# Kernel optimization log

Hardware: AMD Instinct MI355X
Metric: run time of the kernel (lower is better)

Reference implementation:

```python
import jax, jax.numpy as jnp
import numpy as np
import math

N, E, H, A = 50000, 800000, 128, 8
D = H // A


def setup_inputs() -> dict:
    key = jax.random.key(0)
    ks = jax.random.split(key, 12)
    q = jax.random.normal(ks[0], (N, H), dtype=jnp.float32)
    k = jax.random.normal(ks[1], (N, H), dtype=jnp.float32)
    v = jax.random.normal(ks[2], (N, H), dtype=jnp.float32)
    Wq = jax.random.normal(ks[3], (H, H), dtype=jnp.float32) * 0.05
    bq = jax.random.normal(ks[4], (H,), dtype=jnp.float32) * 0.05
    Wk = jax.random.normal(ks[5], (H, H), dtype=jnp.float32) * 0.05
    bk = jax.random.normal(ks[6], (H,), dtype=jnp.float32) * 0.05
    Wv = jax.random.normal(ks[7], (H, H), dtype=jnp.float32) * 0.05
    bv = jax.random.normal(ks[8], (H,), dtype=jnp.float32) * 0.05
    # Ensure every node id appears at least once in q_indices so that
    # q_indices.unique() == arange(N) and the output shape is static [N, H].
    tail = jax.random.randint(ks[9], (E - N,), 0, N)
    q_indices = jnp.concatenate([jnp.arange(N), tail]).astype(jnp.int32)
    k_indices = jax.random.randint(ks[10], (E,), 0, N).astype(jnp.int32)
    return {"q": q, "k": k, "v": v, "Wq": Wq, "bq": bq, "Wk": Wk, "bk": bk,
            "Wv": Wv, "bv": bv, "q_indices": q_indices, "k_indices": k_indices}


def reference(q, k, v, Wq, bq, Wk, bk, Wv, bv, q_indices, k_indices):
    n = q.shape[0]
    # Gather node features per edge (irregular access).
    qe = q[q_indices]            # [E, H]
    ke = k[k_indices]            # [E, H]
    ve = v[k_indices]            # [E, H]
    # Linear projections (torch Linear: x @ W.T + b), split heads -> [E, A, D].
    Q = (qe @ Wq.T + bq).reshape(-1, A, D)
    K = (ke @ Wk.T + bk).reshape(-1, A, D)
    V = (ve @ Wv.T + bv).reshape(-1, A, D)
    # Per-edge scaled dot-product scores: [E, A].
    scores = jnp.einsum('ead,ead->ea', Q, K) / math.sqrt(D)
    # Segment softmax over edges sharing the same destination node
    # (faithful to the original: plain exp, no max subtraction).
    ex = jnp.exp(scores)                                        # [E, A]
    denom = jax.ops.segment_sum(ex, q_indices, num_segments=n)  # [N, A]
    probs = ex / denom[q_indices]                               # [E, A]
    # Scatter-aggregate weighted values per destination node: [N, A, D].
    ctx = jax.ops.segment_sum(probs[:, :, None] * V, q_indices, num_segments=n)
    # Merge heads -> [N, H].
    return ctx.reshape(n, A * D)
```

## Files before the change

### kernel.cpp

```cpp
#include <hip/hip_runtime.h>
#include <hip/hip_bf16.h>

#define HDIM 128
#define OSTR 264

typedef __attribute__((ext_vector_type(8))) short bf16x8;
typedef __attribute__((ext_vector_type(4))) float f32x4;

__device__ inline unsigned short f2bf(float f) {
    return __builtin_bit_cast(unsigned short, __float2bfloat16(f));
}
__device__ inline float bflo(unsigned u) { return __uint_as_float(u << 16); }
__device__ inline float bfhi(unsigned u) { return __uint_as_float(u & 0xffff0000u); }

__device__ inline bf16x8 pack8(float4 a, float4 b) {
    bf16x8 r;
    r[0] = (short)f2bf(a.x); r[1] = (short)f2bf(a.y);
    r[2] = (short)f2bf(a.z); r[3] = (short)f2bf(a.w);
    r[4] = (short)f2bf(b.x); r[5] = (short)f2bf(b.y);
    r[6] = (short)f2bf(b.z); r[7] = (short)f2bf(b.w);
    return r;
}

__global__ void init_kernel(int* __restrict__ deg, int n,
                            const float* __restrict__ Wq, const float* __restrict__ Wk,
                            const float* __restrict__ Wv, unsigned short* __restrict__ Wopt) {
    int i = blockIdx.x * 256 + threadIdx.x;
    if (i < n) deg[i] = 0;
    if (i < 3 * HDIM * HDIM) {
        int j  = i & 7;
        int l  = (i >> 3) & 63;
        int ks = (i >> 9) & 3;
        int nt = (i >> 11) & 7;
        int m  = i >> 14;
        const float* W = (m == 0) ? Wq : (m == 1) ? Wk : Wv;
        int row = nt * 16 + (l & 15);
        int col = ks * 32 + ((l >> 4) << 3) + j;
        Wopt[i] = f2bf(W[row * HDIM + col]);
    }
}

__global__ void proj_deg(const float* __restrict__ qin, const float* __restrict__ kin,
                         const float* __restrict__ vin, const unsigned short* __restrict__ Wopt,
                         const float* __restrict__ bq, const float* __restrict__ bk,
                         const float* __restrict__ bv,
                         unsigned short* __restrict__ Qb, unsigned short* __restrict__ KVb,
                         const int* __restrict__ qidx, int* __restrict__ deg,
                         int* __restrict__ rank, int E, int n, int nbx, int ndeg, int ntot)
{
    __shared__ unsigned short tile[4][16 * OSTR];

    const int id     = blockIdx.x;
    const int before = (int)(((long)id * ndeg) / ntot);
    const bool isdeg = (int)(((long)(id + 1) * ndeg) / ntot) > before;

    if (isdeg) {
        const int e0 = before * 1024 + (int)threadIdx.x * 4;
        if (e0 + 4 <= E) {
            const int4 qi = *(const int4*)&qidx[e0];
            int4 r;
            r.x = atomicAdd(&deg[qi.x], 1);
            r.y = atomicAdd(&deg[qi.y], 1);
            r.z = atomicAdd(&deg[qi.z], 1);
            r.w = atomicAdd(&deg[qi.w], 1);
            *(int4*)&rank[e0] = r;
        } else {
            #pragma unroll
            for (int j = 0; j < 4; ++j)
                if (e0 + j < E) rank[e0 + j] = atomicAdd(&deg[qidx[e0 + j]], 1);
        }
        return;
    }

    const int pid = id - before;
    const bool isQ = (pid < nbx);
    const int bx  = isQ ? pid : (pid - nbx);

    const int tid  = threadIdx.x;
    const int lane = tid & 63;
    const int wv   = tid >> 6;
    const int r15  = lane & 15;
    const int quad = lane >> 4;
    const long node0 = (long)bx * 64;
    const long nodeA = node0 + wv * 16 + r15;
    unsigned short* lq = tile[wv];

#define LOAD_AF(src)                                                           \
    {                                                                          \
        if (nodeA < n) {                                                       \
            const float* xr = (src) + nodeA * HDIM + quad * 8;                 \
            _Pragma("unroll")                                                  \
            for (int ks = 0; ks < 4; ++ks) {                                   \
                float4 lo = *(const float4*)(xr + ks * 32);                    \
                float4 hi = *(const float4*)(xr + ks * 32 + 4);                \
                af[ks] = pack8(lo, hi);                                        \
            }                                                                  \
        } else {                                                               \
            _Pragma("unroll")                                                  \
            for (int ks = 0; ks < 4; ++ks)                                     \
                af[ks] = (bf16x8){0, 0, 0, 0, 0, 0, 0, 0};                     \
        }                                                                      \
    }

#define MFMA_ALL(Wm)                                                           \
    {                                                                          \
        _Pragma("unroll")                                                      \
        for (int nt = 0; nt < 8; ++nt) {                                       \
            acc[nt] = (f32x4){0.f, 0.f, 0.f, 0.f};                             \
            _Pragma("unroll")                                                  \
            for (int ks = 0; ks < 4; ++ks) {                                   \
                const bf16x8 wfrag =                                           \
                    *(const bf16x8*)((Wm) + ((size_t)((nt * 4 + ks) * 64) + lane) * 8); \
                acc[nt] = __builtin_amdgcn_mfma_f32_16x16x32_bf16(af[ks], wfrag, acc[nt], 0, 0, 0); \
            }                                                                  \
        }                                                                      \
    }

    bf16x8 af[4];
    f32x4  acc[8];

    if (isQ) {
        LOAD_AF(qin);
        MFMA_ALL(Wopt);
        #pragma unroll
        for (int nt = 0; nt < 8; ++nt) {
            const int c = nt * 16 + r15;
            const float bias = bq[c];
            #pragma unroll
            for (int r = 0; r < 4; ++r)
                lq[(quad * 4 + r) * OSTR + c] = f2bf(acc[nt][r] + bias);
        }
        #pragma unroll
        for (int it = 0; it < 4; ++it) {
            int g   = it * 64 + lane;
            int row = g >> 4;
            int col = (g & 15) * 8;
            long node = node0 + wv * 16 + row;
            if (node < n) {
                ushort4 lo = *(const ushort4*)&lq[row * OSTR + col];
                ushort4 hi = *(const ushort4*)&lq[row * OSTR + col + 4];
                uint4 o;
                o.x = (unsigned)lo.x | ((unsigned)lo.y << 16);
                o.y = (unsigned)lo.z | ((unsigned)lo.w << 16);
                o.z = (unsigned)hi.x | ((unsigned)hi.y << 16);
                o.w = (unsigned)hi.z | ((unsigned)hi.w << 16);
                *(uint4*)&Qb[node * HDIM + col] = o;
            }
        }
    } else {
        LOAD_AF(kin);
        MFMA_ALL(Wopt + HDIM * HDIM);
        #pragma unroll
        for (int nt = 0; nt < 8; ++nt) {
            const int c = nt * 16 + r15;
            const float bias = bk[c];
            const int  slot = (c >> 2) * 8 + (c & 3);
            #pragma unroll
            for (int r = 0; r < 4; ++r)
                lq[(quad * 4 + r) * OSTR + slot] = f2bf(acc[nt][r] + bias);
        }
        LOAD_AF(vin);
        MFMA_ALL(Wopt + 2 * HDIM * HDIM);
        #pragma unroll
        for (int nt = 0; nt < 8; ++nt) {
            const int c = nt * 16 + r15;
            const float bias = bv[c];
            const int  slot = (c >> 2) * 8 + 4 + (c & 3);
            #pragma unroll
            for (int r = 0; r < 4; ++r)
                lq[(quad * 4 + r) * OSTR + slot] = f2bf(acc[nt][r] + bias);
        }
        #pragma unroll
        for (int it = 0; it < 8; ++it) {
            int g   = it * 64 + lane;
            int row = g >> 5;
            int ch  = g & 31;
            long node = node0 + wv * 16 + row;
            if (node < n)
                *(uint4*)&KVb[(size_t)node * 256 + ch * 8] =
                    *(const uint4*)&lq[row * OSTR + ch * 8];
        }
    }
#undef LOAD_AF
#undef MFMA_ALL
}

__global__ void scan_block(const int* __restrict__ deg, int* __restrict__ offs,
                           int* __restrict__ bsum, int n) {
    __shared__ int ws[17];
    const int tid = threadIdx.x;
    const int lane = tid & 63, wv = tid >> 6;
    int i = blockIdx.x * 1024 + tid;
    int v = (i < n) ? deg[i] : 0;
    int sc = v;
    #pragma unroll
    for (int d = 1; d < 64; d <<= 1) {
        int t = __shfl_up(sc, d, 64);
        if (lane >= d) sc += t;
    }
    if (lane == 63) ws[wv] = sc;
    __syncthreads();
    if (tid == 0) {
        int base = 0;
        #pragma unroll
        for (int w = 0; w < 16; ++w) { int t = ws[w]; ws[w] = base; base += t; }
        ws[16] = base;
    }
    __syncthreads();
    if (i < n) offs[i] = ws[wv] + (sc - v);
    if (tid == 0) bsum[blockIdx.x] = ws[16];
}

__global__ void scan_addtops(const int* __restrict__ bsum, int* __restrict__ offs,
                             int n, int E, int nb) {
    __shared__ int s_base;
    const int tid = threadIdx.x;
    if (tid < 64) {
        int v = (tid < nb) ? bsum[tid] : 0;
        int sc = v;
        #pragma unroll
        for (int d = 1; d < 64; d <<= 1) {
            int t = __shfl_up(sc, d, 64);
            if (tid >= d) sc += t;
        }
        if (tid == blockIdx.x) s_base = sc - v;
    }
    __syncthreads();
    int i = blockIdx.x * 1024 + tid;
    if (i < n) offs[i] += s_base;
    if (blockIdx.x == 0 && tid == 0) offs[n] = E;
}

__global__ void fill_kernel(const int* __restrict__ qidx, const int* __restrict__ kidx,
                            const int* __restrict__ offs, const int* __restrict__ rank,
                            int* __restrict__ srcl, int E) {
    int e0 = (blockIdx.x * 256 + (int)threadIdx.x) * 4;
    if (e0 + 4 <= E) {
        const int4 qi = *(const int4*)&qidx[e0];
        const int4 ki = *(const int4*)&kidx[e0];
        const int4 rk = *(const int4*)&rank[e0];
        srcl[offs[qi.x] + rk.x] = ki.x;
        srcl[offs[qi.y] + rk.y] = ki.y;
        srcl[offs[qi.z] + rk.z] = ki.z;
        srcl[offs[qi.w] + rk.w] = ki.w;
    } else {
        #pragma unroll
        for (int j = 0; j < 4; ++j)
            if (e0 + j < E) srcl[offs[qidx[e0 + j]] + rank[e0 + j]] = kidx[e0 + j];
    }
}

__global__ void agg_kernel(const uint2* __restrict__ Q2, const uint4* __restrict__ KV4,
                           const int* __restrict__ offs, const int* __restrict__ srcl,
                           float* __restrict__ out, int n)
{
    const int tid  = threadIdx.x;
    const int l32  = tid & 31;
    const int node = blockIdx.x * 8 + (tid >> 5);
    if (node >= n) return;

    const uint2 qp = Q2[(size_t)node * 32 + l32];
    const float qx = bflo(qp.x), qy = bfhi(qp.x), qz = bflo(qp.y), qw = bfhi(qp.y);

    float dsum = 0.f, a0 = 0.f, a1 = 0.f, a2 = 0.f, a3 = 0.f;
    const int beg = offs[node], end = offs[node + 1];
    const int srcbase = tid & 32;

#define EDGE_STEP(kv)                                                          \
    {                                                                          \
        float part = qx * bflo((kv).x) + qy * bfhi((kv).x)                     \
                   + qz * bflo((kv).y) + qw * bfhi((kv).y);                    \
        part += __shfl_xor(part, 1, 64);                                       \
        part += __shfl_xor(part, 2, 64);                                       \
        float w = __expf(part * 0.25f);                                        \
        dsum += w;                                                             \
        a0 += w * bflo((kv).z); a1 += w * bfhi((kv).z);                        \
        a2 += w * bflo((kv).w); a3 += w * bfhi((kv).w);                        \
    }

    for (int base = beg; base < end; base += 32) {
        int cnt = min(32, end - base);
        int my = (base + l32 < end) ? srcl[base + l32] : 0;
        int j = 0;
        for (; j + 4 <= cnt; j += 4) {
            int s0 = __shfl(my, srcbase + j,     64);
            int s1 = __shfl(my, srcbase + j + 1, 64);
            int s2 = __shfl(my, srcbase + j + 2, 64);
            int s3 = __shfl(my, srcbase + j + 3, 64);
            uint4 kv0 = KV4[(size_t)s0 * 32 + l32];
            uint4 kv1 = KV4[(size_t)s1 * 32 + l32];
            uint4 kv2 = KV4[(size_t)s2 * 32 + l32];
            uint4 kv3 = KV4[(size_t)s3 * 32 + l32];
            EDGE_STEP(kv0); EDGE_STEP(kv1); EDGE_STEP(kv2); EDGE_STEP(kv3);
        }
        for (; j < cnt; ++j) {
            int s = __shfl(my, srcbase + j, 64);
            uint4 kv = KV4[(size_t)s * 32 + l32];
            EDGE_STEP(kv);
        }
    }
#undef EDGE_STEP

    float inv = 1.f / dsum;
    float4 r = make_float4(a0 * inv, a1 * inv, a2 * inv, a3 * inv);
    *(float4*)&out[(size_t)node * HDIM + l32 * 4] = r;
}

extern "C" void kernel_launch(void* const* d_in, const int* in_sizes, int n_in,
                              void* d_out, int out_size, void* d_ws, size_t ws_size,
                              hipStream_t stream) {
    const float* q  = (const float*)d_in[0];
    const float* k  = (const float*)d_in[1];
    const float* v  = (const float*)d_in[2];
    const float* Wq = (const float*)d_in[3];
    const float* bq = (const float*)d_in[4];
    const float* Wk = (const float*)d_in[5];
    const float* bk = (const float*)d_in[6];
    const float* Wv = (const float*)d_in[7];
    const float* bv = (const float*)d_in[8];
    const int* qidx = (const int*)d_in[9];
    const int* kidx = (const int*)d_in[10];
    float* out = (float*)d_out;

    const int N = in_sizes[0] / HDIM;
    const int E = in_sizes[9];

    char* p = (char*)d_ws;
    unsigned short* Qb  = (unsigned short*)p; p += (size_t)N * HDIM * sizeof(unsigned short);
    unsigned short* KVb = (unsigned short*)p; p += (size_t)2 * N * HDIM * sizeof(unsigned short);
    unsigned short* Wopt = (unsigned short*)p; p += (size_t)3 * HDIM * HDIM * sizeof(unsigned short);
    int* deg  = (int*)p; p += (size_t)N * sizeof(int);
    int* offs = (int*)p; p += (size_t)(N + 1) * sizeof(int);
    int* bsum = (int*)p; p += 64 * sizeof(int);
    int* rank = (int*)p; p += (size_t)E * sizeof(int);
    int* srcl = (int*)p; p += (size_t)E * sizeof(int);

    const int nbx  = (N + 63) / 64;
    const int ndeg = (E + 1023) / 1024;
    const int ntot = 2 * nbx + ndeg;
    const int nfb  = (E + 1023) / 1024;
    const int nb   = (N + 1023) / 1024;
    const int initn = (N > 3 * HDIM * HDIM) ? N : 3 * HDIM * HDIM;

    init_kernel<<<(initn + 255) / 256, 256, 0, stream>>>(deg, N, Wq, Wk, Wv, Wopt);
    proj_deg<<<ntot, 256, 0, stream>>>(q, k, v, Wopt, bq, bk, bv, Qb, KVb,
                                       qidx, deg, rank, E, N, nbx, ndeg, ntot);
    scan_block<<<nb, 1024, 0, stream>>>(deg, offs, bsum, N);
    scan_addtops<<<nb, 1024, 0, stream>>>(bsum, offs, N, E, nb);
    fill_kernel<<<nfb, 256, 0, stream>>>(qidx, kidx, offs, rank, srcl, E);
    agg_kernel<<<(N + 7) / 8, 256, 0, stream>>>((const uint2*)Qb, (const uint4*)KVb,
                                                offs, srcl, out, N);
}
```

Before: 240.8 us.

## Coalesce projection input loads via LDS staging and interleave K/V bf16 pairs

The projection kernel now loads each 64-node input tile with coalesced row-contiguous float4 reads, converts it to bf16 into a shared LDS tile, and then builds the MFMA fragments from LDS. Before, each lane did strided per-row loads straight from global memory. The K and V inputs are both prefetched into registers before either MFMA pass. The output K/V is written in an interleaved (k,v) pair layout, and the aggregation kernel's unpacking is changed to match. This adds several block-wide barriers and higher register pressure in exchange for better global load coalescing in the projection stage.

```diff
diff --git a/kernel.cpp b/kernel.cpp
--- a/kernel.cpp
+++ b/kernel.cpp
@@ -2,6 +2,7 @@
 #include <hip/hip_bf16.h>
 
 #define HDIM 128
+#define ISTR 136
 #define OSTR 264
 
 typedef __attribute__((ext_vector_type(8))) short bf16x8;
@@ -12,15 +13,6 @@
 }
 __device__ inline float bflo(unsigned u) { return __uint_as_float(u << 16); }
 __device__ inline float bfhi(unsigned u) { return __uint_as_float(u & 0xffff0000u); }
-
-__device__ inline bf16x8 pack8(float4 a, float4 b) {
-    bf16x8 r;
-    r[0] = (short)f2bf(a.x); r[1] = (short)f2bf(a.y);
-    r[2] = (short)f2bf(a.z); r[3] = (short)f2bf(a.w);
-    r[4] = (short)f2bf(b.x); r[5] = (short)f2bf(b.y);
-    r[6] = (short)f2bf(b.z); r[7] = (short)f2bf(b.w);
-    return r;
-}
 
 __global__ void init_kernel(int* __restrict__ deg, int n,
                             const float* __restrict__ Wq, const float* __restrict__ Wk,
@@ -48,7 +40,7 @@
                          const int* __restrict__ qidx, int* __restrict__ deg,
                          int* __restrict__ rank, int E, int n, int nbx, int ndeg, int ntot)
 {
-    __shared__ unsigned short tile[4][16 * OSTR];
+    __shared__ unsigned short tile[64 * ISTR];
 
     const int id     = blockIdx.x;
     const int before = (int)(((long)id * ndeg) / ntot);
@@ -82,27 +74,32 @@
     const int r15  = lane & 15;
     const int quad = lane >> 4;
     const long node0 = (long)bx * 64;
-    const long nodeA = node0 + wv * 16 + r15;
-    unsigned short* lq = tile[wv];
-
-#define LOAD_AF(src)                                                           \
+    const int srow = tid >> 5;
+    const int sc4  = tid & 31;
+
+    bf16x8 af[4];
+
+#define STAGE_REGS(dst)                                                        \
     {                                                                          \
-        if (nodeA < n) {                                                       \
-            const float* xr = (src) + nodeA * HDIM + quad * 8;                 \
-            _Pragma("unroll")                                                  \
-            for (int ks = 0; ks < 4; ++ks) {                                   \
-                float4 lo = *(const float4*)(xr + ks * 32);                    \
-                float4 hi = *(const float4*)(xr + ks * 32 + 4);                \
-                af[ks] = pack8(lo, hi);                                        \
-            }                                                                  \
-        } else {                                                               \
-            _Pragma("unroll")                                                  \
-            for (int ks = 0; ks < 4; ++ks)                                     \
-                af[ks] = (bf16x8){0, 0, 0, 0, 0, 0, 0, 0};                     \
+        _Pragma("unroll")                                                      \
+        for (int it = 0; it < 8; ++it) {                                       \
+            int row = srow + it * 8;                                           \
+            float4 val = dst[it];                                              \
+            ushort4 h;                                                         \
+            h.x = f2bf(val.x); h.y = f2bf(val.y);                              \
+            h.z = f2bf(val.z); h.w = f2bf(val.w);                              \
+            *(ushort4*)&tile[row * ISTR + sc4 * 4] = h;                        \
         }                                                                      \
     }
 
-#define MFMA_ALL(Wm)                                                           \
+#define LOAD_FRAGS()                                                           \
+    {                                                                          \
+        _Pragma("unroll")                                                      \
+        for (int ks = 0; ks < 4; ++ks)                                         \
+            af[ks] = *(const bf16x8*)&tile[(wv * 16 + r15) * ISTR + quad * 8 + ks * 32]; \
+    }
+
+#define MFMA_ALL(Wm, acc)                                                      \
     {                                                                          \
         _Pragma("unroll")                                                      \
         for (int nt = 0; nt < 8; ++nt) {                                       \
@@ -116,29 +113,43 @@
         }                                                                      \
     }
 
-    bf16x8 af[4];
-    f32x4  acc[8];
-
     if (isQ) {
-        LOAD_AF(qin);
-        MFMA_ALL(Wopt);
+        #pragma unroll
+        for (int it = 0; it < 8; ++it) {
+            int row = srow + it * 8;
+            long node = node0 + row;
+            float4 val = make_float4(0.f, 0.f, 0.f, 0.f);
+            if (node < n) val = ((const float4*)(qin + node * HDIM))[sc4];
+            ushort4 h;
+            h.x = f2bf(val.x); h.y = f2bf(val.y); h.z = f2bf(val.z); h.w = f2bf(val.w);
+            *(ushort4*)&tile[row * ISTR + sc4 * 4] = h;
+        }
+        __syncthreads();
+
+        f32x4 acc[8];
+        LOAD_FRAGS();
+        MFMA_ALL(Wopt, acc);
+        __syncthreads();
+
         #pragma unroll
         for (int nt = 0; nt < 8; ++nt) {
             const int c = nt * 16 + r15;
             const float bias = bq[c];
             #pragma unroll
             for (int r = 0; r < 4; ++r)
-                lq[(quad * 4 + r) * OSTR + c] = f2bf(acc[nt][r] + bias);
-        }
+                tile[(wv * 16 + quad * 4 + r) * ISTR + c] = f2bf(acc[nt][r] + bias);
+        }
+        __syncthreads();
+
         #pragma unroll
         for (int it = 0; it < 4; ++it) {
-            int g   = it * 64 + lane;
+            int g   = it * 256 + tid;
             int row = g >> 4;
             int col = (g & 15) * 8;
-            long node = node0 + wv * 16 + row;
+            long node = node0 + row;
             if (node < n) {
-                ushort4 lo = *(const ushort4*)&lq[row * OSTR + col];
-                ushort4 hi = *(const ushort4*)&lq[row * OSTR + col + 4];
+                ushort4 lo = *(const ushort4*)&tile[row * ISTR + col];
+                ushort4 hi = *(const ushort4*)&tile[row * ISTR + col + 4];
                 uint4 o;
                 o.x = (unsigned)lo.x | ((unsigned)lo.y << 16);
                 o.y = (unsigned)lo.z | ((unsigned)lo.w << 16);
@@ -148,40 +159,66 @@
             }
         }
     } else {
-        LOAD_AF(kin);
-        MFMA_ALL(Wopt + HDIM * HDIM);
-        #pragma unroll
-        for (int nt = 0; nt < 8; ++nt) {
-            const int c = nt * 16 + r15;
-            const float bias = bk[c];
-            const int  slot = (c >> 2) * 8 + (c & 3);
+        float4 kreg[8], vreg[8];
+        #pragma unroll
+        for (int it = 0; it < 8; ++it) {
+            long node = node0 + srow + it * 8;
+            if (node < n) {
+                kreg[it] = ((const float4*)(kin + node * HDIM))[sc4];
+                vreg[it] = ((const float4*)(vin + node * HDIM))[sc4];
+            } else {
+                kreg[it] = make_float4(0.f, 0.f, 0.f, 0.f);
+                vreg[it] = make_float4(0.f, 0.f, 0.f, 0.f);
+            }
+        }
+
+        f32x4 accK[8], accV[8];
+
+        STAGE_REGS(kreg);
+        __syncthreads();
+        LOAD_FRAGS();
+        MFMA_ALL(Wopt + HDIM * HDIM, accK);
+        __syncthreads();
+
+        STAGE_REGS(vreg);
+        __syncthreads();
+        LOAD_FRAGS();
+        MFMA_ALL(Wopt + 2 * HDIM * HDIM, accV);
+        __syncthreads();
+
+        #pragma unroll
+        for (int h = 0; h < 2; ++h) {
+            if ((wv >> 1) == h) {
+                #pragma unroll
+                for (int nt = 0; nt < 8; ++nt) {
+                    const int c = nt * 16 + r15;
+                    const float bK = bk[c], bV = bv[c];
+                    const int slot = (c >> 2) * 8 + 2 * (c & 3);
+                    #pragma unroll
+                    for (int r = 0; r < 4; ++r) {
+                        const int lr = (wv & 1) * 16 + quad * 4 + r;
+                        unsigned pk = (unsigned)f2bf(accK[nt][r] + bK)
+                                    | ((unsigned)f2bf(accV[nt][r] + bV) << 16);
+                        *(unsigned*)&tile[lr * OSTR + slot] = pk;
+                    }
+                }
+            }
+            __syncthreads();
             #pragma unroll
-            for (int r = 0; r < 4; ++r)
-                lq[(quad * 4 + r) * OSTR + slot] = f2bf(acc[nt][r] + bias);
-        }
-        LOAD_AF(vin);
-        MFMA_ALL(Wopt + 2 * HDIM * HDIM);
-        #pragma unroll
-        for (int nt = 0; nt < 8; ++nt) {
-            const int c = nt * 16 + r15;
-            const float bias = bv[c];
-            const int  slot = (c >> 2) * 8 + 4 + (c & 3);
-            #pragma unroll
-            for (int r = 0; r < 4; ++r)
-                lq[(quad * 4 + r) * OSTR + slot] = f2bf(acc[nt][r] + bias);
-        }
-        #pragma unroll
-        for (int it = 0; it < 8; ++it) {
-            int g   = it * 64 + lane;
-            int row = g >> 5;
-            int ch  = g & 31;
-            long node = node0 + wv * 16 + row;
-            if (node < n)
-                *(uint4*)&KVb[(size_t)node * 256 + ch * 8] =
-                    *(const uint4*)&lq[row * OSTR + ch * 8];
-        }
-    }
-#undef LOAD_AF
+            for (int it = 0; it < 4; ++it) {
+                int g   = it * 256 + tid;
+                int row = g >> 5;
+                int ch  = g & 31;
+                long node = node0 + h * 32 + row;
+                if (node < n)
+                    *(uint4*)&KVb[(size_t)node * 256 + ch * 8] =
+                        *(const uint4*)&tile[row * OSTR + ch * 8];
+            }
+            __syncthreads();
+        }
+    }
+#undef STAGE_REGS
+#undef LOAD_FRAGS
 #undef MFMA_ALL
 }
 
@@ -268,14 +305,14 @@
 
 #define EDGE_STEP(kv)                                                          \
     {                                                                          \
-        float part = qx * bflo((kv).x) + qy * bfhi((kv).x)                     \
-                   + qz * bflo((kv).y) + qw * bfhi((kv).y);                    \
+        float part = qx * bflo((kv).x) + qy * bflo((kv).y)                     \
+                   + qz * bflo((kv).z) + qw * bflo((kv).w);                    \
         part += __shfl_xor(part, 1, 64);                                       \
         part += __shfl_xor(part, 2, 64);                                       \
         float w = __expf(part * 0.25f);                                        \
         dsum += w;                                                             \
-        a0 += w * bflo((kv).z); a1 += w * bfhi((kv).z);                        \
-        a2 += w * bflo((kv).w); a3 += w * bfhi((kv).w);                        \
+        a0 += w * bfhi((kv).x); a1 += w * bfhi((kv).y);                        \
+        a2 += w * bfhi((kv).z); a3 += w * bfhi((kv).w);                        \
     }
 
     for (int base = beg; base < end; base += 32) {
```

New measurement: 243.5 us. No clear change (+1.1%).
